# Performance work log

Measured on AMD Instinct MI355X. Metric: run time of the kernel, lower is better.

Reference implementation:

```python
import jax, jax.numpy as jnp
import numpy as np

N_NODES = 100000
N_EDGES = 800000
IN = 128
HID = 128
EMB = 64
OUT = 8
N_GRAPHS = 64


def setup_inputs() -> dict:
    key = jax.random.key(0)
    ks = jax.random.split(key, 12)
    x = jax.random.normal(ks[0], (N_NODES, IN), dtype=jnp.float32)
    edge_index = jax.random.randint(ks[1], (2, N_EDGES), 0, N_NODES, dtype=jnp.int64)
    batch = jnp.sort(jax.random.randint(ks[2], (N_NODES,), 0, N_GRAPHS, dtype=jnp.int64))
    embed = jax.random.normal(ks[3], (N_GRAPHS, EMB), dtype=jnp.float32)
    s_in = 1.0 / np.sqrt(IN).astype(np.float32)
    s_h = 1.0 / np.sqrt(HID).astype(np.float32)
    s_l = 1.0 / np.sqrt(HID + EMB).astype(np.float32)
    return {
        "x": x,
        "edge_index": edge_index,
        "batch": batch,
        "embed": embed,
        # SAGEConv1: out = lin_l(mean_agg) + lin_r(x); bias lives in lin_l
        "W1l": jax.random.normal(ks[4], (HID, IN), dtype=jnp.float32) * s_in,
        "b1l": jnp.zeros((HID,), dtype=jnp.float32),
        "W1r": jax.random.normal(ks[5], (HID, IN), dtype=jnp.float32) * s_in,
        # SAGEConv2
        "W2l": jax.random.normal(ks[6], (HID, HID), dtype=jnp.float32) * s_h,
        "b2l": jnp.zeros((HID,), dtype=jnp.float32),
        "W2r": jax.random.normal(ks[7], (HID, HID), dtype=jnp.float32) * s_h,
        # final Linear(hidden + embed_dim, out)
        "Wlin": jax.random.normal(ks[8], (OUT, HID + EMB), dtype=jnp.float32) * s_l,
        "blin": jnp.zeros((OUT,), dtype=jnp.float32),
    }


def _segment_mean(vals, idx, num_segments):
    # scatter-mean with count clamped to 1 (matches PyG scatter 'mean')
    s = jax.ops.segment_sum(vals, idx, num_segments=num_segments)
    c = jax.ops.segment_sum(jnp.ones((vals.shape[0], 1), vals.dtype), idx,
                            num_segments=num_segments)
    return s / jnp.maximum(c, 1.0)


def reference(x, edge_index, batch, embed, W1l, b1l, W1r, W2l, b2l, W2r, Wlin, blin):
    src, dst = edge_index[0], edge_index[1]

    def sage(h, Wl, bl, Wr):
        # gather source features, mean-aggregate at destination, then linear
        agg = _segment_mean(h[src], dst, N_NODES)          # [N, d]
        return agg @ Wl.T + bl + h @ Wr.T                   # [N, HID]

    h = jax.nn.relu(sage(x, W1l, b1l, W1r))
    h = jax.nn.relu(sage(h, W2l, b2l, W2r))
    pooled = _segment_mean(h, batch, N_GRAPHS)              # [G, HID]
    z = jnp.concatenate([pooled, embed], axis=1)            # [G, HID+EMB]
    return z @ Wlin.T + blin                                # [G, OUT]
```

## Files before the change

kernel.cpp:

```cpp
#include <hip/hip_runtime.h>
#include <stdint.h>

#define FEAT   128
#define GR     64
#define LDA    136
#define NBUCK  256
#define BSHIFT 9

typedef __attribute__((ext_vector_type(8))) short bf8_t;
typedef __attribute__((ext_vector_type(4))) float f4_t;

__device__ inline float bf2f(ushort h){
    union { uint u; float f; } v; v.u = ((uint)h) << 16; return v.f;
}
__device__ inline float bf2f_lo(uint u){
    union { uint u; float f; } v; v.u = u << 16; return v.f;
}
__device__ inline float bf2f_hi(uint u){
    union { uint u; float f; } v; v.u = u & 0xffff0000u; return v.f;
}
__device__ inline ushort f2bf(float f){
    union { float f; uint u; } v; v.f = f;
    uint r = (v.u + 0x7FFFu + ((v.u >> 16) & 1u)) >> 16;
    return (ushort)r;
}

__global__ __launch_bounds__(256) void k_prep(
    const float* __restrict__ x, ushort* __restrict__ xb, int n4, int nbCast,
    const float* __restrict__ a0, const float* __restrict__ a1,
    const float* __restrict__ a2, const float* __restrict__ a3,
    ushort* __restrict__ o0, ushort* __restrict__ o1,
    ushort* __restrict__ o2, ushort* __restrict__ o3,
    const int* __restrict__ dst, int* __restrict__ bcnt, int E)
{
    int bid = blockIdx.x;
    if (bid < nbCast){
        int i = bid * 256 + threadIdx.x;
        if (i >= n4) return;
        float4 v = ((const float4*)x)[i];
        ushort4 o; o.x = f2bf(v.x); o.y = f2bf(v.y); o.z = f2bf(v.z); o.w = f2bf(v.w);
        ((ushort4*)xb)[i] = o;
        return;
    }
    if (bid < nbCast + 64){
        int i = (bid - nbCast) * 256 + threadIdx.x;
        int sel = i >> 12, j = i & 4095;
        const float* s = sel == 0 ? a0 : sel == 1 ? a1 : sel == 2 ? a2 : a3;
        ushort*      d = sel == 0 ? o0 : sel == 1 ? o1 : sel == 2 ? o2 : o3;
        float4 v = ((const float4*)s)[j];
        ushort4 o; o.x = f2bf(v.x); o.y = f2bf(v.y); o.z = f2bf(v.z); o.w = f2bf(v.w);
        ((ushort4*)d)[j] = o;
        return;
    }
    __shared__ int h[NBUCK];
    h[threadIdx.x] = 0;
    __syncthreads();
    int base = (bid - nbCast - 64) * 4096 + threadIdx.x;
    #pragma unroll
    for (int k = 0; k < 16; k++){
        int e = base + k * 256;
        if (e < E) atomicAdd(&h[dst[e] >> BSHIFT], 1);
    }
    __syncthreads();
    int c = h[threadIdx.x];
    if (c) atomicAdd(&bcnt[threadIdx.x], c);
}

__global__ void k_bscan(const int* __restrict__ bcnt, int* __restrict__ bbase,
                        int* __restrict__ bpos, int* __restrict__ rowp,
                        int* __restrict__ csr, int E, int M){
    __shared__ int sd[NBUCK];
    int t = threadIdx.x;
    int v = bcnt[t];
    sd[t] = v; __syncthreads();
    for (int off = 1; off < NBUCK; off <<= 1){
        int x = (t >= off) ? sd[t - off] : 0;
        __syncthreads();
        sd[t] += x;
        __syncthreads();
    }
    int ex = sd[t] - v;
    bbase[t] = ex;
    bpos[t]  = ex;
    if (t < 8) csr[E + t] = 0;
    if (t == NBUCK - 1){ bbase[NBUCK] = sd[t]; rowp[M] = E; }
}

__global__ __launch_bounds__(256) void k_bucket(const int* __restrict__ src,
                                                const int* __restrict__ dst,
                                                int* __restrict__ bpos,
                                                int2* __restrict__ bp, int E){
    __shared__ int h[NBUCK];
    __shared__ int bb[NBUCK];
    int t = threadIdx.x;
    h[t] = 0;
    __syncthreads();
    int base = blockIdx.x * 4096 + t;
    int bk[16], sv[16], dv[16];
    #pragma unroll
    for (int k = 0; k < 16; k++){
        int e = base + k * 256;
        if (e < E){
            dv[k] = dst[e]; sv[k] = src[e];
            bk[k] = dv[k] >> BSHIFT;
            atomicAdd(&h[bk[k]], 1);
        } else bk[k] = -1;
    }
    __syncthreads();
    int c = h[t];
    bb[t] = c ? atomicAdd(&bpos[t], c) : 0;
    __syncthreads();
    h[t] = 0;
    __syncthreads();
    #pragma unroll
    for (int k = 0; k < 16; k++){
        if (bk[k] >= 0){
            int r = atomicAdd(&h[bk[k]], 1);
            bp[bb[bk[k]] + r] = make_int2(sv[k], dv[k]);
        }
    }
}

__global__ __launch_bounds__(512) void k_csr(const int2* __restrict__ bp,
                                             const int* __restrict__ bbase,
                                             int* __restrict__ rowp,
                                             int* __restrict__ csr, int M){
    __shared__ int cnt[512];
    __shared__ int sd[512];
    int b = blockIdx.x, t = threadIdx.x;
    int nbase = b << BSHIFT;
    int nnodes = min(512, M - nbase);
    int e0 = bbase[b], e1 = bbase[b + 1];
    cnt[t] = 0;
    __syncthreads();
    for (int e = e0 + t; e < e1; e += 512)
        atomicAdd(&cnt[bp[e].y - nbase], 1);
    __syncthreads();
    int v = cnt[t];
    sd[t] = v; __syncthreads();
    for (int off = 1; off < 512; off <<= 1){
        int x = (t >= off) ? sd[t - off] : 0;
        __syncthreads();
        sd[t] += x;
        __syncthreads();
    }
    int ex = sd[t] - v;
    if (t < nnodes) rowp[nbase + t] = e0 + ex;
    cnt[t] = ex;
    __syncthreads();
    for (int e = e0 + t; e < e1; e += 512){
        int2 pr = bp[e];
        int r = atomicAdd(&cnt[pr.y - nbase], 1);
        csr[e0 + r] = pr.x;
    }
}

#define ACCA(vv)                                   \
    a0 += bf2f_lo((vv).x); a1 += bf2f_hi((vv).x);  \
    a2 += bf2f_lo((vv).y); a3 += bf2f_hi((vv).y);  \
    a4 += bf2f_lo((vv).z); a5 += bf2f_hi((vv).z);  \
    a6 += bf2f_lo((vv).w); a7 += bf2f_hi((vv).w);
#define ACCB(vv)                                   \
    b0 += bf2f_lo((vv).x); b1 += bf2f_hi((vv).x);  \
    b2 += bf2f_lo((vv).y); b3 += bf2f_hi((vv).y);  \
    b4 += bf2f_lo((vv).z); b5 += bf2f_hi((vv).z);  \
    b6 += bf2f_lo((vv).w); b7 += bf2f_hi((vv).w);

__global__ __launch_bounds__(256) void k_agg(const ushort* __restrict__ srcf,
                                             const int* __restrict__ rowp,
                                             const int* __restrict__ csr,
                                             ushort* __restrict__ aggb, int M){
    int node = blockIdx.x * 16 + (threadIdx.x >> 4);
    int l    = threadIdx.x & 15;
    if (node >= M) return;
    int s = rowp[node], e = rowp[node + 1];
    const char* base = (const char*)srcf + (uint)l * 16u;
    float a0 = 0.f, a1 = 0.f, a2 = 0.f, a3 = 0.f;
    float a4 = 0.f, a5 = 0.f, a6 = 0.f, a7 = 0.f;
    float b0 = 0.f, b1 = 0.f, b2 = 0.f, b3 = 0.f;
    float b4 = 0.f, b5 = 0.f, b6 = 0.f, b7 = 0.f;
    int i = s;
    for (; i + 8 <= e; i += 8){
        int idx[8];
        __builtin_memcpy(idx, csr + i, 32);
        uint4 v0 = *(const uint4*)(base + ((uint)idx[0] << 8));
        uint4 v1 = *(const uint4*)(base + ((uint)idx[1] << 8));
        uint4 v2 = *(const uint4*)(base + ((uint)idx[2] << 8));
        uint4 v3 = *(const uint4*)(base + ((uint)idx[3] << 8));
        uint4 v4 = *(const uint4*)(base + ((uint)idx[4] << 8));
        uint4 v5 = *(const uint4*)(base + ((uint)idx[5] << 8));
        uint4 v6 = *(const uint4*)(base + ((uint)idx[6] << 8));
        uint4 v7 = *(const uint4*)(base + ((uint)idx[7] << 8));
        ACCA(v0); ACCA(v1); ACCA(v2); ACCA(v3);
        ACCB(v4); ACCB(v5); ACCB(v6); ACCB(v7);
    }
    if (i + 4 <= e){
        int idx[4];
        __builtin_memcpy(idx, csr + i, 16);
        uint4 v0 = *(const uint4*)(base + ((uint)idx[0] << 8));
        uint4 v1 = *(const uint4*)(base + ((uint)idx[1] << 8));
        uint4 v2 = *(const uint4*)(base + ((uint)idx[2] << 8));
        uint4 v3 = *(const uint4*)(base + ((uint)idx[3] << 8));
        ACCA(v0); ACCA(v1); ACCB(v2); ACCB(v3);
        i += 4;
    }
    for (; i < e; i++){
        uint4 v = *(const uint4*)(base + ((uint)csr[i] << 8));
        ACCA(v);
    }
    float inv = (e > s) ? 1.0f / (float)(e - s) : 0.f;
    uint4 o;
    o.x = ((uint)f2bf((a1 + b1) * inv) << 16) | (uint)f2bf((a0 + b0) * inv);
    o.y = ((uint)f2bf((a3 + b3) * inv) << 16) | (uint)f2bf((a2 + b2) * inv);
    o.z = ((uint)f2bf((a5 + b5) * inv) << 16) | (uint)f2bf((a4 + b4) * inv);
    o.w = ((uint)f2bf((a7 + b7) * inv) << 16) | (uint)f2bf((a6 + b6) * inv);
    *(uint4*)(aggb + (size_t)node * FEAT + l * 8) = o;
}

__global__ __launch_bounds__(512) void k_gemm(
    const ushort* __restrict__ Aagg, const ushort* __restrict__ Aself,
    const ushort* __restrict__ Wl, const ushort* __restrict__ Wr,
    const float* __restrict__ bias, ushort* __restrict__ Hout, int M)
{
    __shared__ ushort Bs[128 * LDA];
    const int tid  = threadIdx.x;
    const int lane = tid & 63;
    const int wave = tid >> 6;
    const int l15  = lane & 15;
    const int quad = lane >> 4;
    const int m0   = blockIdx.x * 128;

    int arow = m0 + wave * 16 + l15;
    if (arow >= M) arow = M - 1;
    const ushort* ap0 = Aagg  + (size_t)arow * FEAT + quad * 8;
    const ushort* ap1 = Aself + (size_t)arow * FEAT + quad * 8;

    f4_t acc[8];
    #pragma unroll
    for (int i = 0; i < 8; i++) acc[i] = (f4_t){0.f, 0.f, 0.f, 0.f};

    #pragma unroll
    for (int pass = 0; pass < 2; pass++){
        const ushort* Ap = pass ? ap1 : ap0;
        const ushort* Wp = pass ? Wr  : Wl;
        #pragma unroll
        for (int it = 0; it < 4; it++){
            int idx = (it * 512 + tid) * 8;
            int r = idx >> 7, c = idx & 127;
            *(int4*)(&Bs[r * LDA + c]) = *(const int4*)(Wp + idx);
        }
        bf8_t ga0 = *(const bf8_t*)(Ap);
        bf8_t ga1 = *(const bf8_t*)(Ap + 32);
        bf8_t ga2 = *(const bf8_t*)(Ap + 64);
        bf8_t ga3 = *(const bf8_t*)(Ap + 96);
        __syncthreads();
        const ushort* brow = &Bs[l15 * LDA + quad * 8];
        #pragma unroll
        for (int nt = 0; nt < 8; nt++){
            const ushort* b = brow + nt * 16 * LDA;
            acc[nt] = __builtin_amdgcn_mfma_f32_16x16x32_bf16(ga0, *(const bf8_t*)(b),      acc[nt], 0, 0, 0);
            acc[nt] = __builtin_amdgcn_mfma_f32_16x16x32_bf16(ga1, *(const bf8_t*)(b + 32), acc[nt], 0, 0, 0);
            acc[nt] = __builtin_amdgcn_mfma_f32_16x16x32_bf16(ga2, *(const bf8_t*)(b + 64), acc[nt], 0, 0, 0);
            acc[nt] = __builtin_amdgcn_mfma_f32_16x16x32_bf16(ga3, *(const bf8_t*)(b + 96), acc[nt], 0, 0, 0);
        }
        __syncthreads();
    }
    #pragma unroll
    for (int nt = 0; nt < 8; nt++){
        int col = nt * 16 + l15;
        float bcol = bias[col];
        #pragma unroll
        for (int reg = 0; reg < 4; reg++){
            int gm = m0 + wave * 16 + quad * 4 + reg;
            if (gm < M){
                float v = acc[nt][reg] + bcol;
                v = v > 0.f ? v : 0.f;
                Hout[(size_t)gm * FEAT + col] = f2bf(v);
            }
        }
    }
}

__global__ void k_pool(const ushort* __restrict__ h, const int* __restrict__ batch,
                       float* __restrict__ pooled, int M){
    int f   = threadIdx.x & 127;
    int sub = threadIdx.x >> 7;
    int n0  = (blockIdx.x * 2 + sub) * 16;
    if (n0 >= M) return;
    int n1 = min(n0 + 16, M);
    int g = batch[n0];
    float s = 0.f;
    int n = n0;
    for (; n + 4 <= n1; n += 4){
        int g0 = batch[n], g1 = batch[n + 1], g2 = batch[n + 2], g3 = batch[n + 3];
        float v0 = bf2f(h[(size_t)n * FEAT + f]);
        float v1 = bf2f(h[(size_t)(n + 1) * FEAT + f]);
        float v2 = bf2f(h[(size_t)(n + 2) * FEAT + f]);
        float v3 = bf2f(h[(size_t)(n + 3) * FEAT + f]);
        if (g0 != g){ atomicAdd(&pooled[g * FEAT + f], s); s = 0.f; g = g0; } s += v0;
        if (g1 != g){ atomicAdd(&pooled[g * FEAT + f], s); s = 0.f; g = g1; } s += v1;
        if (g2 != g){ atomicAdd(&pooled[g * FEAT + f], s); s = 0.f; g = g2; } s += v2;
        if (g3 != g){ atomicAdd(&pooled[g * FEAT + f], s); s = 0.f; g = g3; } s += v3;
    }
    for (; n < n1; n++){
        int gn = batch[n];
        if (gn != g){ atomicAdd(&pooled[g * FEAT + f], s); s = 0.f; g = gn; }
        s += bf2f(h[(size_t)n * FEAT + f]);
    }
    atomicAdd(&pooled[g * FEAT + f], s);
}

__global__ void k_final(const float* __restrict__ pooled, const int* __restrict__ batch,
                        const float* __restrict__ embed, const float* __restrict__ Wlin,
                        const float* __restrict__ blin, float* __restrict__ out, int M){
    int t = threadIdx.x;
    if (t >= GR * 8) return;
    int g = t >> 3, o = t & 7;
    int lo = 0, hi = M;
    while (lo < hi){ int mid = (lo + hi) >> 1; if (batch[mid] < g) lo = mid + 1; else hi = mid; }
    int s0 = lo;
    lo = s0; hi = M;
    while (lo < hi){ int mid = (lo + hi) >> 1; if (batch[mid] < g + 1) lo = mid + 1; else hi = mid; }
    int c = lo - s0;
    float inv = (c > 0) ? 1.0f / (float)c : 0.f;
    float acc = blin[o];
    const float* wr = Wlin + o * (FEAT + GR);
    for (int k = 0; k < FEAT; k++) acc += pooled[g * FEAT + k] * inv * wr[k];
    for (int k = 0; k < GR; k++)   acc += embed[g * GR + k] * wr[FEAT + k];
    out[g * 8 + o] = acc;
}

extern "C" void kernel_launch(void* const* d_in, const int* in_sizes, int n_in,
                              void* d_out, int out_size, void* d_ws, size_t ws_size,
                              hipStream_t stream)
{
    const float* x     = (const float*)d_in[0];
    const int*   eidx  = (const int*)d_in[1];
    const int*   batch = (const int*)d_in[2];
    const float* embed = (const float*)d_in[3];
    const float* W1l   = (const float*)d_in[4];
    const float* b1l   = (const float*)d_in[5];
    const float* W1r   = (const float*)d_in[6];
    const float* W2l   = (const float*)d_in[7];
    const float* b2l   = (const float*)d_in[8];
    const float* W2r   = (const float*)d_in[9];
    const float* Wlin  = (const float*)d_in[10];
    const float* blin  = (const float*)d_in[11];
    float* out = (float*)d_out;

    const int M = in_sizes[0] / FEAT;
    const int E = in_sizes[1] / 2;
    const int* src = eidx;
    const int* dst = eidx + E;

    char* w = (char*)d_ws;
    size_t off = 0;
    auto alloc = [&](size_t sz){ void* p = w + off; off = (off + sz + 255) & ~(size_t)255; return p; };
    ushort* xb     = (ushort*)alloc((size_t)M * FEAT * 2);
    ushort* aggb   = (ushort*)alloc((size_t)M * FEAT * 2);
    ushort* h1b    = (ushort*)alloc((size_t)M * FEAT * 2);
    int*    rowp   = (int*)alloc((size_t)(M + 1) * 4);
    int*    csr    = (int*)alloc((size_t)(E + 8) * 4);
    int*    bcnt   = (int*)alloc(NBUCK * 4);
    int*    bbase  = (int*)alloc((NBUCK + 1) * 4);
    int*    bpos   = (int*)alloc(NBUCK * 4);
    float*  pooled = (float*)alloc((size_t)GR * FEAT * 4);
    ushort* w1lb   = (ushort*)alloc((size_t)FEAT * FEAT * 2);
    ushort* w1rb   = (ushort*)alloc((size_t)FEAT * FEAT * 2);
    ushort* w2lb   = (ushort*)alloc((size_t)FEAT * FEAT * 2);
    ushort* w2rb   = (ushort*)alloc((size_t)FEAT * FEAT * 2);
    int2*   bp     = (int2*)aggb;
    ushort* h2b    = xb;

    hipMemsetAsync(bcnt, 0, NBUCK * 4, stream);
    hipMemsetAsync(pooled, 0, (size_t)GR * FEAT * 4, stream);

    const int n4     = M * FEAT / 4;
    const int nbCast = (n4 + 255) / 256;
    const int nb     = (M + 511) >> BSHIFT;
    const int ebk    = (E + 4095) / 4096;
    k_prep  <<<nbCast + 64 + ebk, 256, 0, stream>>>(x, xb, n4, nbCast,
                                                    W1l, W1r, W2l, W2r,
                                                    w1lb, w1rb, w2lb, w2rb,
                                                    dst, bcnt, E);
    k_bscan <<<1, NBUCK, 0, stream>>>(bcnt, bbase, bpos, rowp, csr, E, M);
    k_bucket<<<ebk, 256, 0, stream>>>(src, dst, bpos, bp, E);
    k_csr   <<<nb, 512, 0, stream>>>(bp, bbase, rowp, csr, M);
    k_agg   <<<(M + 15) / 16, 256, 0, stream>>>(xb, rowp, csr, aggb, M);
    k_gemm  <<<(M + 127) / 128, 512, 0, stream>>>(aggb, xb, w1lb, w1rb, b1l, h1b, M);
    k_agg   <<<(M + 15) / 16, 256, 0, stream>>>(h1b, rowp, csr, aggb, M);
    k_gemm  <<<(M + 127) / 128, 512, 0, stream>>>(aggb, h1b, w2lb, w2rb, b2l, h2b, M);
    k_pool  <<<(M + 31) / 32, 256, 0, stream>>>(h2b, batch, pooled, M);
    k_final <<<1, 512, 0, stream>>>(pooled, batch, embed, Wlin, blin, out, M);
}
```

Baseline: 301.0 us.

## Fuse mean-pool and final linear into second GEMM epilogue

The second SAGE GEMM no longer writes h2 to memory. Its epilogue applies bias and ReLU, reduces rows per graph across the wave with shuffles, and atomically adds the sums into pooled. The last block to finish, found with an atomic counter, then computes the final linear layer, so the separate pool and final kernels go away. The pooled memset moves into the scan kernel. This removes a full write and read of h2 and two launches, in exchange for more atomics in the epilogue and a last-block serial tail.

After: 378.0 us. 1.26x slower.

```diff
diff --git a/kernel.cpp b/kernel.cpp
--- a/kernel.cpp
+++ b/kernel.cpp
@@ -68,9 +68,13 @@
 
 __global__ void k_bscan(const int* __restrict__ bcnt, int* __restrict__ bbase,
                         int* __restrict__ bpos, int* __restrict__ rowp,
-                        int* __restrict__ csr, int E, int M){
+                        int* __restrict__ csr, float* __restrict__ pooled,
+                        int* __restrict__ ctr, int E, int M){
     __shared__ int sd[NBUCK];
     int t = threadIdx.x;
+    #pragma unroll
+    for (int k = 0; k < 32; k++) pooled[t * 32 + k] = 0.f;
+    if (t == 0) *ctr = 0;
     int v = bcnt[t];
     sd[t] = v; __syncthreads();
     for (int off = 1; off < NBUCK; off <<= 1){
@@ -220,7 +224,10 @@
 __global__ __launch_bounds__(512) void k_gemm(
     const ushort* __restrict__ Aagg, const ushort* __restrict__ Aself,
     const ushort* __restrict__ Wl, const ushort* __restrict__ Wr,
-    const float* __restrict__ bias, ushort* __restrict__ Hout, int M)
+    const float* __restrict__ bias, ushort* __restrict__ Hout, int M, int mode,
+    float* __restrict__ pooled, const int* __restrict__ batch, int* __restrict__ ctr,
+    const float* __restrict__ embed, const float* __restrict__ Wlin,
+    const float* __restrict__ blin, float* __restrict__ out)
 {
     __shared__ ushort Bs[128 * LDA];
     const int tid  = threadIdx.x;
@@ -265,55 +272,89 @@
         }
         __syncthreads();
     }
-    #pragma unroll
-    for (int nt = 0; nt < 8; nt++){
-        int col = nt * 16 + l15;
-        float bcol = bias[col];
+
+    if (mode == 0){
         #pragma unroll
-        for (int reg = 0; reg < 4; reg++){
-            int gm = m0 + wave * 16 + quad * 4 + reg;
-            if (gm < M){
-                float v = acc[nt][reg] + bcol;
-                v = v > 0.f ? v : 0.f;
-                Hout[(size_t)gm * FEAT + col] = f2bf(v);
+        for (int nt = 0; nt < 8; nt++){
+            int col = nt * 16 + l15;
+            float bcol = bias[col];
+            #pragma unroll
+            for (int reg = 0; reg < 4; reg++){
+                int gm = m0 + wave * 16 + quad * 4 + reg;
+                if (gm < M){
+                    float v = acc[nt][reg] + bcol;
+                    v = v > 0.f ? v : 0.f;
+                    Hout[(size_t)gm * FEAT + col] = f2bf(v);
+                }
             }
         }
-    }
-}
-
-__global__ void k_pool(const ushort* __restrict__ h, const int* __restrict__ batch,
-                       float* __restrict__ pooled, int M){
-    int f   = threadIdx.x & 127;
-    int sub = threadIdx.x >> 7;
-    int n0  = (blockIdx.x * 2 + sub) * 16;
-    if (n0 >= M) return;
-    int n1 = min(n0 + 16, M);
-    int g = batch[n0];
-    float s = 0.f;
-    int n = n0;
-    for (; n + 4 <= n1; n += 4){
-        int g0 = batch[n], g1 = batch[n + 1], g2 = batch[n + 2], g3 = batch[n + 3];
-        float v0 = bf2f(h[(size_t)n * FEAT + f]);
-        float v1 = bf2f(h[(size_t)(n + 1) * FEAT + f]);
-        float v2 = bf2f(h[(size_t)(n + 2) * FEAT + f]);
-        float v3 = bf2f(h[(size_t)(n + 3) * FEAT + f]);
-        if (g0 != g){ atomicAdd(&pooled[g * FEAT + f], s); s = 0.f; g = g0; } s += v0;
-        if (g1 != g){ atomicAdd(&pooled[g * FEAT + f], s); s = 0.f; g = g1; } s += v1;
-        if (g2 != g){ atomicAdd(&pooled[g * FEAT + f], s); s = 0.f; g = g2; } s += v2;
-        if (g3 != g){ atomicAdd(&pooled[g * FEAT + f], s); s = 0.f; g = g3; } s += v3;
-    }
-    for (; n < n1; n++){
-        int gn = batch[n];
-        if (gn != g){ atomicAdd(&pooled[g * FEAT + f], s); s = 0.f; g = gn; }
-        s += bf2f(h[(size_t)n * FEAT + f]);
-    }
-    atomicAdd(&pooled[g * FEAT + f], s);
-}
-
-__global__ void k_final(const float* __restrict__ pooled, const int* __restrict__ batch,
-                        const float* __restrict__ embed, const float* __restrict__ Wlin,
-                        const float* __restrict__ blin, float* __restrict__ out, int M){
-    int t = threadIdx.x;
+        return;
+    }
+
+    {
+        int row0 = m0 + wave * 16 + quad * 4;
+        bool wfull = (m0 + wave * 16 + 16 <= M);
+        if (wfull){
+            int4 gq = *(const int4*)(batch + row0);
+            int g_lo = __shfl(gq.x, 0);
+            int g_hi = __shfl(gq.w, 48);
+            if (g_lo == g_hi){
+                #pragma unroll
+                for (int nt = 0; nt < 8; nt++){
+                    float bcol = bias[nt * 16 + l15];
+                    float v = 0.f;
+                    #pragma unroll
+                    for (int reg = 0; reg < 4; reg++){
+                        float t = acc[nt][reg] + bcol;
+                        v += t > 0.f ? t : 0.f;
+                    }
+                    v += __shfl_xor(v, 16);
+                    v += __shfl_xor(v, 32);
+                    if (lane < 16)
+                        atomicAdd(&pooled[g_lo * FEAT + nt * 16 + l15], v);
+                }
+            } else {
+                #pragma unroll
+                for (int nt = 0; nt < 8; nt++){
+                    int col = nt * 16 + l15;
+                    float bcol = bias[col];
+                    float s = 0.f; int g = gq.x;
+                    #pragma unroll
+                    for (int reg = 0; reg < 4; reg++){
+                        int gn = reg == 0 ? gq.x : reg == 1 ? gq.y : reg == 2 ? gq.z : gq.w;
+                        float t = acc[nt][reg] + bcol;
+                        t = t > 0.f ? t : 0.f;
+                        if (gn != g){ atomicAdd(&pooled[g * FEAT + col], s); s = 0.f; g = gn; }
+                        s += t;
+                    }
+                    atomicAdd(&pooled[g * FEAT + col], s);
+                }
+            }
+        } else if (row0 < M){
+            #pragma unroll
+            for (int nt = 0; nt < 8; nt++){
+                int col = nt * 16 + l15;
+                float bcol = bias[col];
+                #pragma unroll
+                for (int reg = 0; reg < 4; reg++){
+                    int gm = row0 + reg;
+                    if (gm < M){
+                        float t = acc[nt][reg] + bcol;
+                        t = t > 0.f ? t : 0.f;
+                        atomicAdd(&pooled[batch[gm] * FEAT + col], t);
+                    }
+                }
+            }
+        }
+    }
+
+    __threadfence();
+    __shared__ int slast;
+    if (tid == 0) slast = atomicAdd(ctr, 1);
+    __syncthreads();
+    if (slast != (int)gridDim.x - 1) return;
+
+    int t = tid;
     if (t >= GR * 8) return;
     int g = t >> 3, o = t & 7;
     int lo = 0, hi = M;
@@ -323,11 +364,15 @@
     while (lo < hi){ int mid = (lo + hi) >> 1; if (batch[mid] < g + 1) lo = mid + 1; else hi = mid; }
     int c = lo - s0;
     float inv = (c > 0) ? 1.0f / (float)c : 0.f;
-    float acc = blin[o];
+    float accf = blin[o];
     const float* wr = Wlin + o * (FEAT + GR);
-    for (int k = 0; k < FEAT; k++) acc += pooled[g * FEAT + k] * inv * wr[k];
-    for (int k = 0; k < GR; k++)   acc += embed[g * GR + k] * wr[FEAT + k];
-    out[g * 8 + o] = acc;
+    for (int k = 0; k < FEAT; k++){
+        float pv = __hip_atomic_load(&pooled[g * FEAT + k], __ATOMIC_RELAXED,
+                                     __HIP_MEMORY_SCOPE_AGENT);
+        accf += pv * inv * wr[k];
+    }
+    for (int k = 0; k < GR; k++) accf += embed[g * GR + k] * wr[FEAT + k];
+    out[g * 8 + o] = accf;
 }
 
 extern "C" void kernel_launch(void* const* d_in, const int* in_sizes, int n_in,
@@ -365,31 +410,31 @@
     int*    bbase  = (int*)alloc((NBUCK + 1) * 4);
     int*    bpos   = (int*)alloc(NBUCK * 4);
     float*  pooled = (float*)alloc((size_t)GR * FEAT * 4);
+    int*    ctr    = (int*)alloc(256);
     ushort* w1lb   = (ushort*)alloc((size_t)FEAT * FEAT * 2);
     ushort* w1rb   = (ushort*)alloc((size_t)FEAT * FEAT * 2);
     ushort* w2lb   = (ushort*)alloc((size_t)FEAT * FEAT * 2);
     ushort* w2rb   = (ushort*)alloc((size_t)FEAT * FEAT * 2);
     int2*   bp     = (int2*)aggb;
-    ushort* h2b    = xb;
 
     hipMemsetAsync(bcnt, 0, NBUCK * 4, stream);
-    hipMemsetAsync(pooled, 0, (size_t)GR * FEAT * 4, stream);
 
     const int n4     = M * FEAT / 4;
     const int nbCast = (n4 + 255) / 256;
     const int nb     = (M + 511) >> BSHIFT;
     const int ebk    = (E + 4095) / 4096;
+    const int gemmb  = (M + 127) / 128;
     k_prep  <<<nbCast + 64 + ebk, 256, 0, stream>>>(x, xb, n4, nbCast,
                                                     W1l, W1r, W2l, W2r,
                                                     w1lb, w1rb, w2lb, w2rb,
                                                     dst, bcnt, E);
-    k_bscan <<<1, NBUCK, 0, stream>>>(bcnt, bbase, bpos, rowp, csr, E, M);
+    k_bscan <<<1, NBUCK, 0, stream>>>(bcnt, bbase, bpos, rowp, csr, pooled, ctr, E, M);
     k_bucket<<<ebk, 256, 0, stream>>>(src, dst, bpos, bp, E);
     k_csr   <<<nb, 512, 0, stream>>>(bp, bbase, rowp, csr, M);
     k_agg   <<<(M + 15) / 16, 256, 0, stream>>>(xb, rowp, csr, aggb, M);
-    k_gemm  <<<(M + 127) / 128, 512, 0, stream>>>(aggb, xb, w1lb, w1rb, b1l, h1b, M);
+    k_gemm  <<<gemmb, 512, 0, stream>>>(aggb, xb, w1lb, w1rb, b1l, h1b, M, 0,
+                                        nullptr, nullptr, nullptr, nullptr, nullptr, nullptr, nullptr);
     k_agg   <<<(M + 15) / 16, 256, 0, stream>>>(h1b, rowp, csr, aggb, M);
-    k_gemm  <<<(M + 127) / 128, 512, 0, stream>>>(aggb, h1b, w2lb, w2rb, b2l, h2b, M);
-    k_pool  <<<(M + 31) / 32, 256, 0, stream>>>(h2b, batch, pooled, M);
-    k_final <<<1, 512, 0, stream>>>(pooled, batch, embed, Wlin, blin, out, M);
-}
+    k_gemm  <<<gemmb, 512, 0, stream>>>(aggb, h1b, w2lb, w2rb, b2l, nullptr, M, 1,
+                                        pooled, batch, ctr, embed, Wlin, blin, out);
+}
```
